# Performance work log

Measured on AMD Instinct MI355X. Metric: run time of the kernel, lower is better.

## Reference

```python
import jax, jax.numpy as jnp
import numpy as np

# Llama-3-8B-like attention, prefill over B sequences of length S (flattened tokens)
D = 4096      # hidden_size
N = 32        # num query heads
K = 8         # num KV heads (GQA)
H = 128       # head_dim (== head_dim_original, already a multiple of 128 so no padding)
B = 4         # sequences in the ragged batch
S = 1024      # tokens per sequence
T = B * S     # total flattened tokens
ROPE_THETA = 10000.0


def _apply_rope(x, positions, head_dim, theta):
    # x: [T, n_heads, H]; positions: [T] int
    inv_freq = 1.0 / (theta ** (jnp.arange(0, head_dim, 2, dtype=jnp.float32) / head_dim))
    freqs = positions.astype(jnp.float32)[:, None] * inv_freq[None, :]  # [T, H/2]
    emb = jnp.concatenate([freqs, freqs], axis=-1)                       # [T, H]
    cos = jnp.cos(emb)[:, None, :].astype(x.dtype)
    sin = jnp.sin(emb)[:, None, :].astype(x.dtype)
    x1, x2 = jnp.split(x, 2, axis=-1)
    rotated = jnp.concatenate([-x2, x1], axis=-1)
    return x * cos + rotated * sin


def setup_inputs() -> dict:
    key = jax.random.key(0)
    ks = jax.random.split(key, 5)
    x = jax.random.normal(ks[0], (T, D), dtype=jnp.float32)
    # positions restart per sequence (ragged prefill metadata)
    input_positions = (jnp.arange(T, dtype=jnp.int32) % S)
    w_scale = 0.02
    Wq = jax.random.normal(ks[1], (D, N, H), dtype=jnp.float32) * w_scale
    Wk = jax.random.normal(ks[2], (D, K, H), dtype=jnp.float32) * w_scale
    Wv = jax.random.normal(ks[3], (D, K, H), dtype=jnp.float32) * w_scale
    Wo = jax.random.normal(ks[4], (N, H, D), dtype=jnp.float32) * w_scale
    return {"x": x, "input_positions": input_positions,
            "Wq": Wq, "Wk": Wk, "Wv": Wv, "Wo": Wo}


def reference(x, input_positions, Wq, Wk, Wv, Wo):
    # QKV projections (flattened tokens)
    q = jnp.einsum('td,dnh->tnh', x, Wq)   # [T, N, H]
    k = jnp.einsum('td,dkh->tkh', x, Wk)   # [T, K, H]
    v = jnp.einsum('td,dkh->tkh', x, Wv)   # [T, K, H]
    q = _apply_rope(q, input_positions, H, ROPE_THETA)
    k = _apply_rope(k, input_positions, H, ROPE_THETA)

    # Ragged causal attention: per-sequence causal SDPA with GQA head grouping.
    G = N // K  # query heads per KV head
    qb = q.reshape(B, S, K, G, H)
    kb = k.reshape(B, S, K, H)
    vb = v.reshape(B, S, K, H)
    scale = jnp.asarray(H, q.dtype) ** -0.5  # head_dim_original ** -0.5
    scores = jnp.einsum('bqkgh,bskh->bkgqs', qb, kb) * scale  # [B,K,G,S,S]
    causal = jnp.tril(jnp.ones((S, S), dtype=bool))
    scores = jnp.where(causal, scores, jnp.finfo(scores.dtype).min)
    probs = jax.nn.softmax(scores, axis=-1)
    out = jnp.einsum('bkgqs,bskh->bqkgh', probs, vb).reshape(T, N, H)

    # Output projection
    o = jnp.einsum('tnh,nhd->td', out, Wo)  # [T, D]
    return o
```

## Files before the change

kernel.cpp:

```cpp
#include <hip/hip_runtime.h>
#include <cstdint>


typedef unsigned short u16;
typedef short bf16x8 __attribute__((ext_vector_type(8)));
typedef float f32x4 __attribute__((ext_vector_type(4)));

#define L2E 1.44269504088896340736f

static __device__ __forceinline__ u16 f2bf(float f) {
  union { float f; unsigned u; } v; v.f = f;
  unsigned r = (v.u + 0x7fffu + ((v.u >> 16) & 1u)) >> 16;
  return (u16)r;
}
static __device__ __forceinline__ float bf2f(u16 h) {
  union { unsigned u; float f; } v; v.u = ((unsigned)h) << 16;
  return v.f;
}

typedef __attribute__((address_space(1))) const unsigned int gas_u32;
typedef __attribute__((address_space(3))) unsigned int las_u32;
static __device__ __forceinline__ void glds16(const void* g, const void* l) {
  __builtin_amdgcn_global_load_lds((gas_u32*)(uintptr_t)g,
                                   (las_u32*)(unsigned)(uintptr_t)l, 16, 0, 0);
}

__global__ __launch_bounds__(256) void cvt_kernel(const float4* __restrict__ in,
                                                  uint2* __restrict__ out, int n4) {
  int i = blockIdx.x * 256 + threadIdx.x;
  if (i < n4) {
    float4 v = in[i];
    uint2 r;
    r.x = (unsigned)f2bf(v.x) | ((unsigned)f2bf(v.y) << 16);
    r.y = (unsigned)f2bf(v.z) | ((unsigned)f2bf(v.w) << 16);
    out[i] = r;
  }
}

__global__ __launch_bounds__(256) void tcvt_kernel(const float* __restrict__ in,
                                                   u16* __restrict__ out, int R, int C) {
  __shared__ float tile[32][33];
  int tx = threadIdx.x, ty = threadIdx.y;
  int r0 = blockIdx.y * 32, c0 = blockIdx.x * 32;
#pragma unroll
  for (int j = 0; j < 4; ++j)
    tile[ty + j * 8][tx] = in[(size_t)(r0 + ty + j * 8) * C + c0 + tx];
  __syncthreads();
#pragma unroll
  for (int j = 0; j < 4; ++j)
    out[(size_t)(c0 + ty + j * 8) * R + r0 + tx] = f2bf(tile[tx][ty + j * 8]);
}

template <int BF16OUT>
__global__ __launch_bounds__(512, 2) void gemm_nt8(const u16* __restrict__ A,
                                                   const u16* __restrict__ Bm,
                                                   void* __restrict__ Cp,
                                                   int M, int N, int Kd) {
  __shared__ u16 Als[2][2][8192];
  __shared__ u16 Bls[2][2][8192];
  const int tid = threadIdx.x;
  const int w = tid >> 6, lane = tid & 63;
  const int ln15 = lane & 15, quad = lane >> 4;
  const int wm = w & 1, wn = w >> 1;

  const int nbm = M >> 8;
  const int nwg = nbm * (N >> 8);
  const int cpx = nwg >> 3;
  const int bid = blockIdx.x;
  const int swz = (bid & 7) * cpx + (bid >> 3);
  const int bm = swz & (nbm - 1);
  const int bn = swz / nbm;
  const int m0 = bm << 8, n0 = bn << 8;

  const int nt = Kd >> 6;

  const int srow = lane >> 2;
  const int schk = ((lane & 3) ^ ((lane >> 3) & 3)) << 3;
  const u16* aSrc = A + (size_t)(m0 + w * 32 + srow) * Kd + schk;
  const u16* bSrc = Bm + (size_t)(n0 + w * 32 + srow) * Kd + schk;
  const int ldsb = w * 1024;

  const int rswz = (quad ^ ((ln15 >> 1) & 3)) << 3;
  const int aoff = (wm * 128 + ln15) * 32 + rswz;
  const int boff = (wn * 64 + ln15) * 32 + rswz;
  const unsigned aAddr = (unsigned)(uintptr_t)&Als[0][0][aoff];
  const unsigned bAddr = (unsigned)(uintptr_t)&Bls[0][0][boff];

  f32x4 acc[8][4];
#pragma unroll
  for (int i = 0; i < 8; ++i)
#pragma unroll
    for (int j = 0; j < 4; ++j) acc[i][j] = f32x4{0.f, 0.f, 0.f, 0.f};
  bf16x8 af[8];

#define DSR(dst, addr, off) \
  asm volatile("ds_read_b128 %0, %1 offset:%2" : "=v"(dst) : "v"(addr), "i"(off))

#define STA(kt, buf, ks)                                          \
  do {                                                            \
    int kc_ = (kt) < nt ? (kt) : nt - 1;                          \
    const u16* s_ = aSrc + (size_t)kc_ * 64 + (ks) * 32;          \
    glds16(s_, &Als[buf][ks][ldsb]);                              \
    glds16(s_ + (size_t)16 * Kd, &Als[buf][ks][ldsb + 512]);      \
  } while (0)
#define STB(kt, buf, ks)                                          \
  do {                                                            \
    int kc_ = (kt) < nt ? (kt) : nt - 1;                          \
    const u16* s_ = bSrc + (size_t)kc_ * 64 + (ks) * 32;          \
    glds16(s_, &Bls[buf][ks][ldsb]);                              \
    glds16(s_ + (size_t)16 * Kd, &Bls[buf][ks][ldsb + 512]);      \
  } while (0)

#define PHASE(buf, ks, nh, STAGE, VM)                                              \
  do {                                                                             \
    if ((nh) == 0) {                                                               \
      DSR(af[0], aAddr, (buf)*32768 + (ks)*16384 + 0 * 1024);                      \
      DSR(af[1], aAddr, (buf)*32768 + (ks)*16384 + 1 * 1024);                      \
      DSR(af[2], aAddr, (buf)*32768 + (ks)*16384 + 2 * 1024);                      \
      DSR(af[3], aAddr, (buf)*32768 + (ks)*16384 + 3 * 1024);                      \
      DSR(af[4], aAddr, (buf)*32768 + (ks)*16384 + 4 * 1024);                      \
      DSR(af[5], aAddr, (buf)*32768 + (ks)*16384 + 5 * 1024);                      \
      DSR(af[6], aAddr, (buf)*32768 + (ks)*16384 + 6 * 1024);                      \
      DSR(af[7], aAddr, (buf)*32768 + (ks)*16384 + 7 * 1024);                      \
    }                                                                              \
    bf16x8 b0_, b1_;                                                               \
    DSR(b0_, bAddr, (buf)*32768 + (ks)*16384 + (nh)*2048);                         \
    DSR(b1_, bAddr, (buf)*32768 + (ks)*16384 + (nh)*2048 + 1024);                  \
    STAGE;                                                                         \
    __builtin_amdgcn_s_barrier();                                                  \
    asm volatile("s_waitcnt lgkmcnt(0)" ::: "memory");                             \
    __builtin_amdgcn_sched_barrier(0);                                             \
    __builtin_amdgcn_s_setprio(1);                                                 \
    _Pragma("unroll") for (int m_ = 0; m_ < 8; ++m_) {                             \
      acc[m_][2 * (nh)] =                                                          \
          __builtin_amdgcn_mfma_f32_16x16x32_bf16(af[m_], b0_, acc[m_][2 * (nh)],  \
                                                  0, 0, 0);                        \
      acc[m_][2 * (nh) + 1] = __builtin_amdgcn_mfma_f32_16x16x32_bf16(             \
          af[m_], b1_, acc[m_][2 * (nh) + 1], 0, 0, 0);                            \
    }                                                                              \
    __builtin_amdgcn_s_setprio(0);                                                 \
    if (VM) asm volatile("s_waitcnt vmcnt(6)" ::: "memory");                       \
    __builtin_amdgcn_s_barrier();                                                  \
    __builtin_amdgcn_sched_barrier(0);                                             \
  } while (0)

  STA(0, 0, 0); STB(0, 0, 0); STA(0, 0, 1); STB(0, 0, 1);
  STA(1, 1, 0); STB(1, 1, 0); STA(1, 1, 1);
  asm volatile("s_waitcnt vmcnt(6)" ::: "memory");
  __builtin_amdgcn_s_barrier();
  __builtin_amdgcn_sched_barrier(0);

  const int iters = nt >> 1;
  for (int i = 0; i < iters; ++i) {
    const int t = 2 * i;
    PHASE(0, 0, 0, STB(t + 1, 1, 1), 0);
    PHASE(0, 0, 1, STA(t + 2, 0, 0), 0);
    PHASE(0, 1, 0, STB(t + 2, 0, 0), 0);
    PHASE(0, 1, 1, STA(t + 2, 0, 1), 1);
    PHASE(1, 0, 0, STB(t + 2, 0, 1), 0);
    PHASE(1, 0, 1, STA(t + 3, 1, 0), 0);
    PHASE(1, 1, 0, STB(t + 3, 1, 0), 0);
    PHASE(1, 1, 1, STA(t + 3, 1, 1), 1);
  }
#undef PHASE
#undef STA
#undef STB
#undef DSR

  const int crow = m0 + wm * 128 + quad * 4;
  const int ccol = n0 + wn * 64 + ln15;
#pragma unroll
  for (int m = 0; m < 8; ++m)
#pragma unroll
    for (int j = 0; j < 4; ++j)
#pragma unroll
      for (int r = 0; r < 4; ++r) {
        float v = acc[m][j][r];
        if (BF16OUT)
          ((u16*)Cp)[(size_t)(crow + m * 16 + r) * N + ccol + j * 16] = f2bf(v);
        else
          ((float*)Cp)[(size_t)(crow + m * 16 + r) * N + ccol + j * 16] = v;
      }
}

__global__ __launch_bounds__(256) void ropetab_kernel(float2* __restrict__ tab) {
  int idx = blockIdx.x * 256 + threadIdx.x;
  int i = idx & 63;
  float inv = exp2f(-0.20751874963942190927f * (float)i);
  float f = (float)(idx >> 6) * inv;
  float s, c;
  sincosf(f, &s, &c);
  tab[idx] = make_float2(c, s);
}

__global__ __launch_bounds__(256) void rope_kernel(u16* __restrict__ qkv,
                                                   const int* __restrict__ pos,
                                                   const float2* __restrict__ tab,
                                                   int total) {
  int idx = blockIdx.x * 256 + threadIdx.x;
  if (idx >= total) return;
  int t = idx / 2560;
  int rem = idx - t * 2560;
  int head = rem >> 6;
  int i = rem & 63;
  float2 cs = tab[(pos[t] << 6) | i];
  float c = cs.x, s = cs.y;
  int colbase = (head < 32) ? head * 128 : (4096 + (head - 32) * 128);
  u16* base = qkv + (size_t)t * 6144 + colbase;
  float x1 = bf2f(base[i]), x2 = bf2f(base[i + 64]);
  float o1 = x1 * c - x2 * s;
  float o2 = x2 * c + x1 * s;
  if (head < 32) { o1 *= 0.08838834764831845f; o2 *= 0.08838834764831845f; }
  base[i] = f2bf(o1);
  base[i + 64] = f2bf(o2);
}

__global__ __launch_bounds__(512, 2) void attn_kernel(const u16* __restrict__ qkv,
                                                      u16* __restrict__ outp) {
  __shared__ u16 Klds[2][64 * 128];
  __shared__ u16 Vtlds[128 * 72];
  __shared__ u16 Plds[8 * 32 * 72];

  const int bx = blockIdx.x;
  const int qb = 15 - (bx >> 5);
  const int kh = bx & 7;
  const int b = (bx >> 3) & 3;

  const int tid = threadIdx.x;
  const int w = tid >> 6;
  const int lane = tid & 63;
  const int ln15 = lane & 15;
  const int quad = lane >> 4;
  const int g = w & 3;
  const int half = w >> 2;
  const int n = kh * 4 + g;

  const int ldq = 6144;
  const int seq0 = b << 10;
  const int q0 = seq0 + qb * 64;

  const u16* Qg = qkv + n * 128;
  const u16* Kg = qkv + 4096 + kh * 128;
  const u16* Vg = qkv + 5120 + kh * 128;

  bf16x8 qf[2][4];
#pragma unroll
  for (int rf = 0; rf < 2; ++rf) {
    const u16* qrow = Qg + (size_t)(q0 + half * 32 + rf * 16 + ln15) * ldq + quad * 8;
#pragma unroll
    for (int ks = 0; ks < 4; ++ks) qf[rf][ks] = *(const bf16x8*)(qrow + ks * 32);
  }

  f32x4 o[2][8];
#pragma unroll
  for (int rf = 0; rf < 2; ++rf)
#pragma unroll
    for (int i = 0; i < 8; ++i) o[rf][i] = f32x4{0.f, 0.f, 0.f, 0.f};
  float m_r[2][4], l_r[2][4];
#pragma unroll
  for (int rf = 0; rf < 2; ++rf)
#pragma unroll
    for (int r = 0; r < 4; ++r) { m_r[rf][r] = -INFINITY; l_r[rf][r] = 0.f; }

  const int kr0 = w * 8 + (lane >> 4);
  const int kr1 = kr0 + 4;
  const u16* kp0 = Kg + (size_t)(seq0 + kr0) * ldq + (((lane & 15) ^ (kr0 & 7)) << 3);
  const u16* kp1 = Kg + (size_t)(seq0 + kr1) * ldq + (((lane & 15) ^ (kr1 & 7)) << 3);

  const int vs0 = (tid & 31) * 2;
  const int vhb = (tid >> 5) * 8;

  union V8 { uint4 v; u16 s[8]; };
  V8 ra, rb;
  {
    const u16* v0 = Vg + (size_t)(seq0 + vs0) * ldq + vhb;
    ra.v = *(const uint4*)v0;
    rb.v = *(const uint4*)(v0 + ldq);
    glds16(kp0, &Klds[0][(w * 8) * 128]);
    glds16(kp1, &Klds[0][(w * 8 + 4) * 128]);
  }

  for (int kt = 0; kt <= qb; ++kt) {
    const int cur = kt & 1;
    __syncthreads();
    {
#pragma unroll
      for (int j = 0; j < 8; ++j) {
        unsigned pk = (unsigned)ra.s[j] | ((unsigned)rb.s[j] << 16);
        *(unsigned*)&Vtlds[(vhb + j) * 72 + vs0] = pk;
      }
    }
    __syncthreads();

    if (kt < qb) {
      glds16(kp0 + (size_t)(kt + 1) * 64 * ldq, &Klds[cur ^ 1][(w * 8) * 128]);
      glds16(kp1 + (size_t)(kt + 1) * 64 * ldq, &Klds[cur ^ 1][(w * 8 + 4) * 128]);
      const u16* v0 = Vg + (size_t)(seq0 + (kt + 1) * 64 + vs0) * ldq + vhb;
      ra.v = *(const uint4*)v0;
      rb.v = *(const uint4*)(v0 + ldq);
    }

    f32x4 sfr[2][4];
#pragma unroll
    for (int rf = 0; rf < 2; ++rf)
#pragma unroll
      for (int c = 0; c < 4; ++c) {
        f32x4 acc = f32x4{0.f, 0.f, 0.f, 0.f};
#pragma unroll
        for (int ks = 0; ks < 4; ++ks) {
          int rr = c * 16 + ln15;
          int ph = (ks * 4 + quad) ^ (rr & 7);
          bf16x8 kf = *(const bf16x8*)&Klds[cur][rr * 128 + ph * 8];
          acc = __builtin_amdgcn_mfma_f32_16x16x32_bf16(qf[rf][ks], kf, acc, 0, 0, 0);
        }
        sfr[rf][c] = acc;
      }

    if (kt == qb) {
#pragma unroll
      for (int rf = 0; rf < 2; ++rf)
#pragma unroll
        for (int c = 0; c < 4; ++c) {
          int col = c * 16 + ln15;
#pragma unroll
          for (int r = 0; r < 4; ++r)
            if (col > half * 32 + rf * 16 + quad * 4 + r) sfr[rf][c][r] = -INFINITY;
        }
    }

    float mx[2][4];
#pragma unroll
    for (int rf = 0; rf < 2; ++rf)
#pragma unroll
      for (int r = 0; r < 4; ++r) {
        float m0 = fmaxf(fmaxf(sfr[rf][0][r], sfr[rf][1][r]),
                         fmaxf(sfr[rf][2][r], sfr[rf][3][r]));
        m0 = fmaxf(m0, __shfl_xor(m0, 1));
        m0 = fmaxf(m0, __shfl_xor(m0, 2));
        m0 = fmaxf(m0, __shfl_xor(m0, 4));
        m0 = fmaxf(m0, __shfl_xor(m0, 8));
        mx[rf][r] = m0;
      }
    float ex = -INFINITY;
#pragma unroll
    for (int rf = 0; rf < 2; ++rf)
#pragma unroll
      for (int r = 0; r < 4; ++r) ex = fmaxf(ex, mx[rf][r] - m_r[rf][r]);
    if (!__all(ex <= 8.f)) {
#pragma unroll
      for (int rf = 0; rf < 2; ++rf)
#pragma unroll
        for (int r = 0; r < 4; ++r) {
          float mnew = fmaxf(m_r[rf][r], mx[rf][r]);
          float al = exp2f((m_r[rf][r] - mnew) * L2E);
          m_r[rf][r] = mnew;
          l_r[rf][r] *= al;
#pragma unroll
          for (int ht = 0; ht < 8; ++ht) o[rf][ht][r] *= al;
        }
    }
#pragma unroll
    for (int rf = 0; rf < 2; ++rf)
#pragma unroll
      for (int r = 0; r < 4; ++r) {
        float rs = 0.f;
#pragma unroll
        for (int c = 0; c < 4; ++c) {
          float pv = exp2f((sfr[rf][c][r] - m_r[rf][r]) * L2E);
          sfr[rf][c][r] = pv;
          rs += pv;
        }
        rs += __shfl_xor(rs, 1);
        rs += __shfl_xor(rs, 2);
        rs += __shfl_xor(rs, 4);
        rs += __shfl_xor(rs, 8);
        l_r[rf][r] += rs;
      }

#pragma unroll
    for (int rf = 0; rf < 2; ++rf)
#pragma unroll
      for (int c = 0; c < 4; ++c)
#pragma unroll
        for (int r = 0; r < 4; ++r)
          Plds[w * 2304 + (rf * 16 + quad * 4 + r) * 72 + c * 16 + ln15] =
              f2bf(sfr[rf][c][r]);

    asm volatile("s_waitcnt lgkmcnt(0)" ::: "memory");

    bf16x8 pf[2][2];
#pragma unroll
    for (int rf = 0; rf < 2; ++rf)
#pragma unroll
      for (int ks = 0; ks < 2; ++ks)
        pf[rf][ks] =
            *(const bf16x8*)&Plds[w * 2304 + (rf * 16 + ln15) * 72 + ks * 32 + quad * 8];
#pragma unroll
    for (int ht = 0; ht < 8; ++ht)
#pragma unroll
      for (int ks = 0; ks < 2; ++ks) {
        bf16x8 vf = *(const bf16x8*)&Vtlds[(ht * 16 + ln15) * 72 + ks * 32 + quad * 8];
#pragma unroll
        for (int rf = 0; rf < 2; ++rf)
          o[rf][ht] = __builtin_amdgcn_mfma_f32_16x16x32_bf16(pf[rf][ks], vf, o[rf][ht],
                                                              0, 0, 0);
      }
  }

#pragma unroll
  for (int rf = 0; rf < 2; ++rf)
#pragma unroll
    for (int r = 0; r < 4; ++r) l_r[rf][r] = 1.f / l_r[rf][r];
#pragma unroll
  for (int rf = 0; rf < 2; ++rf)
#pragma unroll
    for (int ht = 0; ht < 8; ++ht)
#pragma unroll
      for (int r = 0; r < 4; ++r)
        outp[(size_t)(q0 + half * 32 + rf * 16 + quad * 4 + r) * 4096 + n * 128 +
             ht * 16 + ln15] = f2bf(o[rf][ht][r] * l_r[rf][r]);
}

extern "C" void kernel_launch(void* const* d_in, const int* in_sizes, int n_in,
                              void* d_out, int out_size, void* d_ws, size_t ws_size,
                              hipStream_t stream) {
  const float* x = (const float*)d_in[0];
  const int* posi = (const int*)d_in[1];
  const float* Wq = (const float*)d_in[2];
  const float* Wk = (const float*)d_in[3];
  const float* Wv = (const float*)d_in[4];
  const float* Wo = (const float*)d_in[5];
  float* out = (float*)d_out;
  char* ws = (char*)d_ws;

  u16* xb = (u16*)(ws);
  u16* Wt = (u16*)(ws + 33554432);
  u16* WoT = (u16*)(ws + 83886080);
  u16* qkv = (u16*)(ws + 117440512);
  u16* attn = xb;
  float2* rtab = (float2*)ws;

  cvt_kernel<<<16384, 256, 0, stream>>>((const float4*)x, (uint2*)xb, 4194304);
  tcvt_kernel<<<dim3(128, 128), dim3(32, 8), 0, stream>>>(Wq, Wt, 4096, 4096);
  tcvt_kernel<<<dim3(32, 128), dim3(32, 8), 0, stream>>>(Wk, Wt + (size_t)4096 * 4096, 4096, 1024);
  tcvt_kernel<<<dim3(32, 128), dim3(32, 8), 0, stream>>>(Wv, Wt + (size_t)5120 * 4096, 4096, 1024);
  tcvt_kernel<<<dim3(128, 128), dim3(32, 8), 0, stream>>>(Wo, WoT, 4096, 4096);

  gemm_nt8<1><<<dim3(384), 512, 0, stream>>>(xb, Wt, qkv, 4096, 6144, 4096);
  ropetab_kernel<<<256, 256, 0, stream>>>(rtab);
  rope_kernel<<<40960, 256, 0, stream>>>(qkv, posi, rtab, 10485760);
  attn_kernel<<<512, 512, 0, stream>>>(qkv, attn);
  gemm_nt8<0><<<dim3(256), 512, 0, stream>>>(attn, WoT, out, 4096, 4096, 4096);
}
```

Baseline: 687.6 us.

## Fuse RoPE into QKV GEMM epilogue and vectorize weight transpose-convert

```diff
diff --git a/kernel.cpp b/kernel.cpp
--- a/kernel.cpp
+++ b/kernel.cpp
@@ -39,23 +39,44 @@
 
 __global__ __launch_bounds__(256) void tcvt_kernel(const float* __restrict__ in,
                                                    u16* __restrict__ out, int R, int C) {
-  __shared__ float tile[32][33];
-  int tx = threadIdx.x, ty = threadIdx.y;
-  int r0 = blockIdx.y * 32, c0 = blockIdx.x * 32;
-#pragma unroll
-  for (int j = 0; j < 4; ++j)
-    tile[ty + j * 8][tx] = in[(size_t)(r0 + ty + j * 8) * C + c0 + tx];
+  __shared__ float tile[64][68];
+  int tx = threadIdx.x & 15, ty = threadIdx.x >> 4;
+  int r0 = blockIdx.y * 64, c0 = blockIdx.x * 64;
+#pragma unroll
+  for (int k = 0; k < 4; ++k) {
+    float4 v = *(const float4*)&in[(size_t)(r0 + ty + k * 16) * C + c0 + tx * 4];
+    *(float4*)&tile[ty + k * 16][tx * 4] = v;
+  }
   __syncthreads();
 #pragma unroll
-  for (int j = 0; j < 4; ++j)
-    out[(size_t)(c0 + ty + j * 8) * R + r0 + tx] = f2bf(tile[tx][ty + j * 8]);
-}
-
-template <int BF16OUT>
+  for (int k = 0; k < 4; ++k) {
+    int ocol = ty + k * 16;
+    ushort4 o;
+    o.x = f2bf(tile[tx * 4 + 0][ocol]);
+    o.y = f2bf(tile[tx * 4 + 1][ocol]);
+    o.z = f2bf(tile[tx * 4 + 2][ocol]);
+    o.w = f2bf(tile[tx * 4 + 3][ocol]);
+    *(ushort4*)&out[(size_t)(c0 + ocol) * R + r0 + tx * 4] = o;
+  }
+}
+
+__global__ __launch_bounds__(256) void ropetab_kernel(float2* __restrict__ tab) {
+  int idx = blockIdx.x * 256 + threadIdx.x;
+  int i = idx & 63;
+  float inv = exp2f(-0.20751874963942190927f * (float)i);
+  float f = (float)(idx >> 6) * inv;
+  float s, c;
+  sincosf(f, &s, &c);
+  tab[idx] = make_float2(c, s);
+}
+
+template <int BF16OUT, int ROPE>
 __global__ __launch_bounds__(512, 2) void gemm_nt8(const u16* __restrict__ A,
                                                    const u16* __restrict__ Bm,
                                                    void* __restrict__ Cp,
-                                                   int M, int N, int Kd) {
+                                                   int M, int N, int Kd,
+                                                   const int* __restrict__ posi,
+                                                   const float2* __restrict__ rtab) {
   __shared__ u16 Als[2][2][8192];
   __shared__ u16 Bls[2][2][8192];
   const int tid = threadIdx.x;
@@ -82,7 +103,7 @@
 
   const int rswz = (quad ^ ((ln15 >> 1) & 3)) << 3;
   const int aoff = (wm * 128 + ln15) * 32 + rswz;
-  const int boff = (wn * 64 + ln15) * 32 + rswz;
+  const int boff = ((wn >> 1) * 128 + (wn & 1) * 32 + ln15) * 32 + rswz;
   const unsigned aAddr = (unsigned)(uintptr_t)&Als[0][0][aoff];
   const unsigned bAddr = (unsigned)(uintptr_t)&Bls[0][0][boff];
 
@@ -124,8 +145,8 @@
       DSR(af[7], aAddr, (buf)*32768 + (ks)*16384 + 7 * 1024);                      \
     }                                                                              \
     bf16x8 b0_, b1_;                                                               \
-    DSR(b0_, bAddr, (buf)*32768 + (ks)*16384 + (nh)*2048);                         \
-    DSR(b1_, bAddr, (buf)*32768 + (ks)*16384 + (nh)*2048 + 1024);                  \
+    DSR(b0_, bAddr, (buf)*32768 + (ks)*16384 + (nh)*4096);                         \
+    DSR(b1_, bAddr, (buf)*32768 + (ks)*16384 + (nh)*4096 + 1024);                  \
     STAGE;                                                                         \
     __builtin_amdgcn_s_barrier();                                                  \
     asm volatile("s_waitcnt lgkmcnt(0)" ::: "memory");                             \
@@ -168,51 +189,44 @@
 #undef DSR
 
   const int crow = m0 + wm * 128 + quad * 4;
-  const int ccol = n0 + wn * 64 + ln15;
-#pragma unroll
-  for (int m = 0; m < 8; ++m)
-#pragma unroll
-    for (int j = 0; j < 4; ++j)
+  const int ccol = n0 + (wn >> 1) * 128 + (wn & 1) * 32 + ln15;
+  const int cat = (n0 < 4096) ? 0 : (n0 < 5120 ? 1 : 2);
+
+  if (ROPE && cat < 2) {
+    const float qs = (cat == 0) ? 0.08838834764831845f : 1.0f;
+    const int i0 = (wn & 1) * 32 + ln15;
+#pragma unroll
+    for (int m = 0; m < 8; ++m)
 #pragma unroll
       for (int r = 0; r < 4; ++r) {
-        float v = acc[m][j][r];
-        if (BF16OUT)
-          ((u16*)Cp)[(size_t)(crow + m * 16 + r) * N + ccol + j * 16] = f2bf(v);
-        else
-          ((float*)Cp)[(size_t)(crow + m * 16 + r) * N + ccol + j * 16] = v;
-      }
-}
-
-__global__ __launch_bounds__(256) void ropetab_kernel(float2* __restrict__ tab) {
-  int idx = blockIdx.x * 256 + threadIdx.x;
-  int i = idx & 63;
-  float inv = exp2f(-0.20751874963942190927f * (float)i);
-  float f = (float)(idx >> 6) * inv;
-  float s, c;
-  sincosf(f, &s, &c);
-  tab[idx] = make_float2(c, s);
-}
-
-__global__ __launch_bounds__(256) void rope_kernel(u16* __restrict__ qkv,
-                                                   const int* __restrict__ pos,
-                                                   const float2* __restrict__ tab,
-                                                   int total) {
-  int idx = blockIdx.x * 256 + threadIdx.x;
-  if (idx >= total) return;
-  int t = idx / 2560;
-  int rem = idx - t * 2560;
-  int head = rem >> 6;
-  int i = rem & 63;
-  float2 cs = tab[(pos[t] << 6) | i];
-  float c = cs.x, s = cs.y;
-  int colbase = (head < 32) ? head * 128 : (4096 + (head - 32) * 128);
-  u16* base = qkv + (size_t)t * 6144 + colbase;
-  float x1 = bf2f(base[i]), x2 = bf2f(base[i + 64]);
-  float o1 = x1 * c - x2 * s;
-  float o2 = x2 * c + x1 * s;
-  if (head < 32) { o1 *= 0.08838834764831845f; o2 *= 0.08838834764831845f; }
-  base[i] = f2bf(o1);
-  base[i + 64] = f2bf(o2);
+        int row = crow + m * 16 + r;
+        int p = posi[row];
+#pragma unroll
+        for (int s = 0; s < 2; ++s) {
+          float2 cs = rtab[(p << 6) + i0 + s * 16];
+          float x1 = acc[m][s][r], x2 = acc[m][s + 2][r];
+          float o1 = (x1 * cs.x - x2 * cs.y) * qs;
+          float o2 = (x2 * cs.x + x1 * cs.y) * qs;
+          ((u16*)Cp)[(size_t)row * N + ccol + s * 16] = f2bf(o1);
+          ((u16*)Cp)[(size_t)row * N + ccol + s * 16 + 64] = f2bf(o2);
+        }
+      }
+  } else {
+#pragma unroll
+    for (int m = 0; m < 8; ++m)
+#pragma unroll
+      for (int j = 0; j < 4; ++j) {
+        int col = ccol + (j & 1) * 16 + (j >> 1) * 64;
+#pragma unroll
+        for (int r = 0; r < 4; ++r) {
+          float v = acc[m][j][r];
+          if (BF16OUT)
+            ((u16*)Cp)[(size_t)(crow + m * 16 + r) * N + col] = f2bf(v);
+          else
+            ((float*)Cp)[(size_t)(crow + m * 16 + r) * N + col] = v;
+        }
+      }
+  }
 }
 
 __global__ __launch_bounds__(512, 2) void attn_kernel(const u16* __restrict__ qkv,
@@ -438,17 +452,17 @@
   u16* WoT = (u16*)(ws + 83886080);
   u16* qkv = (u16*)(ws + 117440512);
   u16* attn = xb;
-  float2* rtab = (float2*)ws;
+  float2* rtab = (float2*)d_out;
 
   cvt_kernel<<<16384, 256, 0, stream>>>((const float4*)x, (uint2*)xb, 4194304);
-  tcvt_kernel<<<dim3(128, 128), dim3(32, 8), 0, stream>>>(Wq, Wt, 4096, 4096);
-  tcvt_kernel<<<dim3(32, 128), dim3(32, 8), 0, stream>>>(Wk, Wt + (size_t)4096 * 4096, 4096, 1024);
-  tcvt_kernel<<<dim3(32, 128), dim3(32, 8), 0, stream>>>(Wv, Wt + (size_t)5120 * 4096, 4096, 1024);
-  tcvt_kernel<<<dim3(128, 128), dim3(32, 8), 0, stream>>>(Wo, WoT, 4096, 4096);
-
-  gemm_nt8<1><<<dim3(384), 512, 0, stream>>>(xb, Wt, qkv, 4096, 6144, 4096);
+  tcvt_kernel<<<dim3(64, 64), 256, 0, stream>>>(Wq, Wt, 4096, 4096);
+  tcvt_kernel<<<dim3(16, 64), 256, 0, stream>>>(Wk, Wt + (size_t)4096 * 4096, 4096, 1024);
+  tcvt_kernel<<<dim3(16, 64), 256, 0, stream>>>(Wv, Wt + (size_t)5120 * 4096, 4096, 1024);
+  tcvt_kernel<<<dim3(64, 64), 256, 0, stream>>>(Wo, WoT, 4096, 4096);
   ropetab_kernel<<<256, 256, 0, stream>>>(rtab);
-  rope_kernel<<<40960, 256, 0, stream>>>(qkv, posi, rtab, 10485760);
+
+  gemm_nt8<1, 1><<<dim3(384), 512, 0, stream>>>(xb, Wt, qkv, 4096, 6144, 4096, posi, rtab);
   attn_kernel<<<512, 512, 0, stream>>>(qkv, attn);
-  gemm_nt8<0><<<dim3(256), 512, 0, stream>>>(attn, WoT, out, 4096, 4096, 4096);
-}
+  gemm_nt8<0, 0><<<dim3(256), 512, 0, stream>>>(attn, WoT, out, 4096, 4096, 4096,
+                                                nullptr, nullptr);
+}
```

Result: faster. 665.9 us (-3.2%).
